# Kernel tuning notes

Hardware: AMD Instinct MI355X
Metric: run time of the kernel (lower is better)

Reference implementation:

```python
import jax, jax.numpy as jnp
import numpy as np

NUM_EXPERTS = 8
TOP_K = 2


def setup_inputs() -> dict:
    key = jax.random.key(0)
    k0, k1, k2, k3, k4 = jax.random.split(key, 5)
    T, D, F, E = 4096, 2048, 4096, NUM_EXPERTS  # tokens, hidden, intermediate, experts
    s_in = 1.0 / np.sqrt(D).astype(np.float32)
    s_mid = 1.0 / np.sqrt(F).astype(np.float32)
    return {
        "hidden_states": jax.random.normal(k0, (T, D), jnp.float32),
        "gate_w": jax.random.normal(k1, (D, E), jnp.float32) * s_in,   # router gate (no bias)
        "w1": jax.random.normal(k2, (E, D, F), jnp.float32) * s_in,     # expert gate proj
        "w3": jax.random.normal(k3, (E, D, F), jnp.float32) * s_in,     # expert up proj
        "w2": jax.random.normal(k4, (E, F, D), jnp.float32) * s_mid,    # expert down proj
    }


def reference(hidden_states, gate_w, w1, w3, w2):
    x = hidden_states  # [T, D] (original flattens any leading dims)
    # Router: logits in fp32 (router_logits.float()), softmax over ALL experts,
    # take top-k WITHOUT renormalization (renormalize=False).
    logits = (x @ gate_w).astype(jnp.float32)            # [T, E]
    probs = jax.nn.softmax(logits, axis=-1)              # [T, E]
    topk_w, topk_i = jax.lax.top_k(probs, TOP_K)         # [T, K]
    # Dense combine weights: zero for non-selected experts. [T, E]
    combine = jnp.sum(
        jax.nn.one_hot(topk_i, NUM_EXPERTS, dtype=x.dtype) * topk_w[..., None],
        axis=1,
    )

    # SwiGLU experts, vmapped over the expert axis (fixed, small E).
    def expert_fn(w1e, w3e, w2e):
        return (jax.nn.silu(x @ w1e) * (x @ w3e)) @ w2e  # [T, D]

    expert_out = jax.vmap(expert_fn)(w1, w3, w2)         # [E, T, D]
    return jnp.einsum("te,etd->td", combine, expert_out)  # [T, D]
```

## Files before the change

kernel.cpp:

```cpp
#include <hip/hip_runtime.h>
#include <hip/hip_bf16.h>

#define TK 4096
#define DD 2048
#define FF 4096
#define NE 8
#define BM 128
#define BN 128
#define BN2 256
#define BKR 32
#define BKP 64

typedef __attribute__((ext_vector_type(8))) short bf16x8;
typedef __attribute__((ext_vector_type(4))) short bf16x4;
typedef __attribute__((ext_vector_type(4))) float f32x4;

__device__ __forceinline__ unsigned short f2bf(float f) {
  return __builtin_bit_cast(unsigned short, __float2bfloat16(f));
}
__device__ __forceinline__ float bf2f(unsigned short u) {
  return __builtin_bit_cast(float, (unsigned)u << 16);
}

__device__ __forceinline__ void gl16(const unsigned short* g, unsigned short* l) {
  __builtin_amdgcn_global_load_lds(
      (const __attribute__((address_space(1))) unsigned int*)g,
      (__attribute__((address_space(3))) unsigned int*)l, 16, 0, 0);
}

#define VMCNT(n) asm volatile("s_waitcnt vmcnt(" #n ")" ::: "memory")
#define SBAR()   __builtin_amdgcn_s_barrier()

__device__ __forceinline__ int g_swz(int row) { return ((row >> 1) & 3) ^ ((row >> 3) & 3); }
__device__ __forceinline__ int swzoff(int row, int bir) {
  return row * 64 + ((((bir >> 4) ^ g_swz(row)) & 3) << 4) + (bir & 15);
}
__device__ __forceinline__ int permB(int f) {
  return (f & 0x60) | ((f & 3) << 3) | ((f >> 2) & 7);
}

__global__ void k_router(const float* __restrict__ x, const float* __restrict__ gw,
                         int* __restrict__ cnt, int* __restrict__ ltok,
                         float* __restrict__ lw, unsigned short* __restrict__ xb,
                         int2* __restrict__ t2s) {
  int tok = (blockIdx.x * blockDim.x + threadIdx.x) >> 6;
  int lane = threadIdx.x & 63;
  if (tok >= TK) return;
  const float* xr = x + (size_t)tok * DD;
  float a0=0,a1=0,a2=0,a3=0,a4=0,a5=0,a6=0,a7=0;
  for (int p = 0; p < DD / 256; ++p) {
    int d0 = p * 256 + lane * 4;
    f32x4 xv = *(const f32x4*)(xr + d0);
    if (xb) {
      bf16x4 t;
      t[0] = (short)f2bf(xv[0]); t[1] = (short)f2bf(xv[1]);
      t[2] = (short)f2bf(xv[2]); t[3] = (short)f2bf(xv[3]);
      *(bf16x4*)(xb + (size_t)tok * DD + d0) = t;
    }
#pragma unroll
    for (int j = 0; j < 4; ++j) {
      float xs = xv[j];
      const f32x4* g = (const f32x4*)(gw + (size_t)(d0 + j) * NE);
      f32x4 g0 = g[0], g1 = g[1];
      a0 += xs * g0[0]; a1 += xs * g0[1]; a2 += xs * g0[2]; a3 += xs * g0[3];
      a4 += xs * g1[0]; a5 += xs * g1[1]; a6 += xs * g1[2]; a7 += xs * g1[3];
    }
  }
#pragma unroll
  for (int s = 32; s > 0; s >>= 1) {
    a0 += __shfl_xor(a0, s, 64); a1 += __shfl_xor(a1, s, 64);
    a2 += __shfl_xor(a2, s, 64); a3 += __shfl_xor(a3, s, 64);
    a4 += __shfl_xor(a4, s, 64); a5 += __shfl_xor(a5, s, 64);
    a6 += __shfl_xor(a6, s, 64); a7 += __shfl_xor(a7, s, 64);
  }
  if (lane == 0) {
    float p_[NE] = {a0, a1, a2, a3, a4, a5, a6, a7};
    float m = p_[0];
#pragma unroll
    for (int e = 1; e < NE; ++e) m = fmaxf(m, p_[e]);
    float ssum = 0.f;
#pragma unroll
    for (int e = 0; e < NE; ++e) { p_[e] = __expf(p_[e] - m); ssum += p_[e]; }
    float inv = 1.f / ssum;
    int i1 = 0; float b1 = p_[0];
#pragma unroll
    for (int e = 1; e < NE; ++e) if (p_[e] > b1) { b1 = p_[e]; i1 = e; }
    int i2 = -1; float b2 = -1.f;
#pragma unroll
    for (int e = 0; e < NE; ++e) if (e != i1 && p_[e] > b2) { b2 = p_[e]; i2 = e; }
    int s1 = atomicAdd(&cnt[i1], 1);
    ltok[i1 * TK + s1] = tok; lw[i1 * TK + s1] = b1 * inv;
    int s2 = atomicAdd(&cnt[i2], 1);
    ltok[i2 * TK + s2] = tok; lw[i2 * TK + s2] = b2 * inv;
    if (t2s) t2s[tok] = make_int2(i1 * TK + s1, i2 * TK + s2);
  }
}

__global__ void k_prefix(const int* __restrict__ cnt, int* __restrict__ off) {
  if (threadIdx.x == 0) {
    int a = 0;
#pragma unroll
    for (int e = 0; e < NE; ++e) { off[e] = a; a += cnt[e]; }
    off[NE] = a;
  }
}

__global__ __launch_bounds__(256)
void k_tr(const float* __restrict__ src0, unsigned short* __restrict__ dst0,
          int R, int C) {
  const int e = blockIdx.z;
  const float* src = src0 + (size_t)e * R * C;
  unsigned short* dst = dst0 + (size_t)e * R * C;
  const int tid = threadIdx.x;
  const int w = tid >> 6, lane = tid & 63;
  const int r0 = blockIdx.y * 256 + w * 64 + (lane >> 3) * 8;
  const int c0 = blockIdx.x * 32 + (lane & 7) * 4;
  f32x4 v[8];
#pragma unroll
  for (int j = 0; j < 8; ++j) v[j] = *(const f32x4*)(src + (size_t)(r0 + j) * C + c0);
#pragma unroll
  for (int jc = 0; jc < 4; ++jc) {
    bf16x8 o;
#pragma unroll
    for (int j = 0; j < 8; ++j) o[j] = (short)f2bf(v[j][jc]);
    *(bf16x8*)(dst + (size_t)(c0 + jc) * R + r0) = o;
  }
}

__global__ __launch_bounds__(256)
void k_comb(const unsigned short* __restrict__ O, const int2* __restrict__ t2s,
            const int* __restrict__ off, float* __restrict__ out) {
  const int idx = blockIdx.x * 256 + threadIdx.x;
  const int t = idx >> 8;
  const int d0 = (idx & 255) * 8;
  const int2 v = t2s[t];
  const int s1 = off[v.x >> 12] + (v.x & (TK - 1));
  const int s2 = off[v.y >> 12] + (v.y & (TK - 1));
  bf16x8 a = *(const bf16x8*)(O + (size_t)s1 * DD + d0);
  bf16x8 b = *(const bf16x8*)(O + (size_t)s2 * DD + d0);
  f32x4 r0, r1;
#pragma unroll
  for (int j = 0; j < 4; ++j) {
    r0[j] = bf2f((unsigned short)a[j]) + bf2f((unsigned short)b[j]);
    r1[j] = bf2f((unsigned short)a[j + 4]) + bf2f((unsigned short)b[j + 4]);
  }
  float* o = out + (size_t)t * DD + d0;
  *(f32x4*)o = r0;
  *(f32x4*)(o + 4) = r1;
}


__global__ __launch_bounds__(256, 2)
void k_gemm1g(const unsigned short* __restrict__ xb, const unsigned short* __restrict__ w1t,
              const unsigned short* __restrict__ w3t, const int* __restrict__ cnt,
              const int* __restrict__ off, const int* __restrict__ ltok,
              const float* __restrict__ lw, unsigned short* __restrict__ H) {
  const int e = blockIdx.z;
  const int ce = cnt[e];
  const int m0 = blockIdx.y * BM;
  if (m0 >= ce) return;
  const int n0 = blockIdx.x * BN;
  const int tid = threadIdx.x, lane = tid & 63, w = tid >> 6;
  const int wr = w >> 1, wc = w & 1;
  const unsigned short* W1 = w1t + (size_t)e * FF * DD;
  const unsigned short* W3 = w3t + (size_t)e * FF * DD;
  const int base = off[e];

  __shared__ __align__(16) unsigned short As[BM * BKP];
  __shared__ __align__(16) unsigned short B1s[2][BM * BKP];
  __shared__ __align__(16) unsigned short B3s[2][BM * BKP];

  const int swz8 = ((lane & 7) ^ ((lane >> 3) & 7)) * 8;
  const unsigned short *aSrc[4], *b1Src[4], *b3Src[4];
#pragma unroll
  for (int i = 0; i < 4; ++i) {
    int row = w * 32 + i * 8 + (lane >> 3);
    int gm = m0 + row;
    int tok = (gm < ce) ? ltok[e * TK + gm] : ltok[e * TK];
    aSrc[i]  = xb + (size_t)tok * DD + swz8;
    b1Src[i] = W1 + (size_t)(n0 + row) * DD + swz8;
    b3Src[i] = W3 + (size_t)(n0 + row) * DD + swz8;
  }

  const int kc = lane >> 4;
  int aOff[4][2], bOff[4][2];
#pragma unroll
  for (int m = 0; m < 4; ++m) {
    int row = wr * 64 + m * 16 + (lane & 15);
#pragma unroll
    for (int kk = 0; kk < 2; ++kk) {
      int c = kk * 4 + kc;
      aOff[m][kk] = row * 128 + ((c ^ (row & 7)) << 4);
    }
  }
#pragma unroll
  for (int n = 0; n < 4; ++n) {
    int row = wc * 64 + n * 16 + (lane & 15);
#pragma unroll
    for (int kk = 0; kk < 2; ++kk) {
      int c = kk * 4 + kc;
      bOff[n][kk] = row * 128 + ((c ^ (row & 7)) << 4);
    }
  }

  f32x4 acc1[4][4], acc3[4][4];
#pragma unroll
  for (int m = 0; m < 4; ++m)
#pragma unroll
    for (int n = 0; n < 4; ++n)
#pragma unroll
      for (int j = 0; j < 4; ++j) { acc1[m][n][j] = 0.f; acc3[m][n][j] = 0.f; }

  auto STAGE_A = [&]() {
#pragma unroll
    for (int i = 0; i < 4; ++i) {
      gl16(aSrc[i], &As[(w * 4 + i) * 512]);
      aSrc[i] += BKP;
    }
  };
  auto STAGE_B = [&](int buf) {
#pragma unroll
    for (int i = 0; i < 4; ++i) {
      const int seg = w * 4 + i;
      gl16(b1Src[i], &B1s[buf][seg * 512]);
      gl16(b3Src[i], &B3s[buf][seg * 512]);
      b1Src[i] += BKP; b3Src[i] += BKP;
    }
  };
  auto COMPUTE = [&](int buf) {
#pragma unroll
    for (int kk = 0; kk < 2; ++kk) {
      bf16x8 af[4];
#pragma unroll
      for (int m = 0; m < 4; ++m) af[m] = *(const bf16x8*)((const char*)As + aOff[m][kk]);
#pragma unroll
      for (int n = 0; n < 4; ++n) {
        bf16x8 b1 = *(const bf16x8*)((const char*)B1s[buf] + bOff[n][kk]);
        bf16x8 b3 = *(const bf16x8*)((const char*)B3s[buf] + bOff[n][kk]);
#pragma unroll
        for (int m = 0; m < 4; ++m) {
          acc1[m][n] = __builtin_amdgcn_mfma_f32_16x16x32_bf16(af[m], b1, acc1[m][n], 0, 0, 0);
          acc3[m][n] = __builtin_amdgcn_mfma_f32_16x16x32_bf16(af[m], b3, acc3[m][n], 0, 0, 0);
        }
      }
    }
  };

  const int NT = DD / BKP;
  STAGE_A();
  STAGE_B(0);
  int b = 0;
  for (int kt = 0; kt < NT - 1; ++kt) {
    STAGE_B(b ^ 1);
    VMCNT(8);
    SBAR();
    COMPUTE(b);
    SBAR();
    STAGE_A();
    b ^= 1;
  }
  VMCNT(0);
  SBAR();
  COMPUTE(b);

#pragma unroll
  for (int m = 0; m < 4; ++m) {
    const int rbase = wr * 64 + m * 16 + ((lane >> 4) << 2);
    float wts[4]; bool val[4];
#pragma unroll
    for (int j = 0; j < 4; ++j) {
      int r = m0 + rbase + j;
      val[j] = r < ce;
      wts[j] = val[j] ? lw[e * TK + r] : 0.f;
    }
#pragma unroll
    for (int n = 0; n < 4; ++n) {
      const int col = n0 + wc * 64 + n * 16 + (lane & 15);
#pragma unroll
      for (int j = 0; j < 4; ++j) {
        if (!val[j]) continue;
        float s1 = acc1[m][n][j], s3 = acc3[m][n][j];
        float h = s1 / (1.f + __expf(-s1)) * s3 * wts[j];
        H[(size_t)(base + m0 + rbase + j) * FF + col] = f2bf(h);
      }
    }
  }
}

__global__ __launch_bounds__(256, 2)
void k_gemm2g(const unsigned short* __restrict__ H, const unsigned short* __restrict__ w2t,
              const int* __restrict__ cnt, const int* __restrict__ off,
              unsigned short* __restrict__ O) {
  const int e = blockIdx.z;
  const int ce = cnt[e];
  const int m0 = blockIdx.y * BM;
  if (m0 >= ce) return;
  const int n0 = blockIdx.x * BN2;
  const int tid = threadIdx.x, lane = tid & 63, w = tid >> 6;
  const int wr = w >> 1, wc = w & 1;
  const unsigned short* W2 = w2t + (size_t)e * DD * FF;
  const int base = off[e];

  __shared__ __align__(16) unsigned short As[BM * BKP];
  __shared__ __align__(16) unsigned short Bs[2][BN2 * BKP];

  const int swz8 = ((lane & 7) ^ ((lane >> 3) & 7)) * 8;
  const unsigned short *aSrc[4], *bSrc[8];
#pragma unroll
  for (int i = 0; i < 4; ++i) {
    int row = w * 32 + i * 8 + (lane >> 3);
    int gm = m0 + row;
    int hr = (gm < ce) ? gm : 0;
    aSrc[i] = H + (size_t)(base + hr) * FF + swz8;
  }
#pragma unroll
  for (int i = 0; i < 8; ++i) {
    int row = w * 64 + i * 8 + (lane >> 3);
    bSrc[i] = W2 + (size_t)(n0 + row) * FF + swz8;
  }

  const int kc = lane >> 4;
  int aOff[4][2], bOff[8][2];
#pragma unroll
  for (int m = 0; m < 4; ++m) {
    int row = wr * 64 + m * 16 + (lane & 15);
#pragma unroll
    for (int kk = 0; kk < 2; ++kk) {
      int c = kk * 4 + kc;
      aOff[m][kk] = row * 128 + ((c ^ (row & 7)) << 4);
    }
  }
#pragma unroll
  for (int n = 0; n < 8; ++n) {
    int row = wc * 128 + n * 16 + (lane & 15);
#pragma unroll
    for (int kk = 0; kk < 2; ++kk) {
      int c = kk * 4 + kc;
      bOff[n][kk] = row * 128 + ((c ^ (row & 7)) << 4);
    }
  }

  f32x4 acc[4][8];
#pragma unroll
  for (int m = 0; m < 4; ++m)
#pragma unroll
    for (int n = 0; n < 8; ++n)
#pragma unroll
      for (int j = 0; j < 4; ++j) acc[m][n][j] = 0.f;

  auto STAGE_A = [&]() {
#pragma unroll
    for (int i = 0; i < 4; ++i) {
      gl16(aSrc[i], &As[(w * 4 + i) * 512]);
      aSrc[i] += BKP;
    }
  };
  auto STAGE_B = [&](int buf) {
#pragma unroll
    for (int i = 0; i < 8; ++i) {
      gl16(bSrc[i], &Bs[buf][(w * 8 + i) * 512]);
      bSrc[i] += BKP;
    }
  };
  auto COMPUTE = [&](int buf) {
#pragma unroll
    for (int kk = 0; kk < 2; ++kk) {
      bf16x8 af[4];
#pragma unroll
      for (int m = 0; m < 4; ++m) af[m] = *(const bf16x8*)((const char*)As + aOff[m][kk]);
#pragma unroll
      for (int n = 0; n < 8; ++n) {
        bf16x8 bf = *(const bf16x8*)((const char*)Bs[buf] + bOff[n][kk]);
#pragma unroll
        for (int m = 0; m < 4; ++m)
          acc[m][n] = __builtin_amdgcn_mfma_f32_16x16x32_bf16(af[m], bf, acc[m][n], 0, 0, 0);
      }
    }
  };

  const int NT = FF / BKP;
  STAGE_A();
  STAGE_B(0);
  int b = 0;
  for (int kt = 0; kt < NT - 1; ++kt) {
    STAGE_B(b ^ 1);
    VMCNT(8);
    SBAR();
    COMPUTE(b);
    SBAR();
    STAGE_A();
    b ^= 1;
  }
  VMCNT(0);
  SBAR();
  COMPUTE(b);

#pragma unroll
  for (int m = 0; m < 4; ++m) {
    const int rbase = wr * 64 + m * 16 + ((lane >> 4) << 2);
#pragma unroll
    for (int n = 0; n < 8; ++n) {
      const int col = n0 + wc * 128 + n * 16 + (lane & 15);
#pragma unroll
      for (int j = 0; j < 4; ++j) {
        int r = m0 + rbase + j;
        if (r < ce) O[(size_t)(base + r) * DD + col] = f2bf(acc[m][n][j]);
      }
    }
  }
}

__global__ __launch_bounds__(256, 2)
void k_gemm1(const float* __restrict__ x, const float* __restrict__ w1g,
             const float* __restrict__ w3g, const int* __restrict__ cnt,
             const int* __restrict__ off, const int* __restrict__ ltok,
             const float* __restrict__ lw, unsigned short* __restrict__ H) {
  const int e = blockIdx.z;
  const int ce = cnt[e];
  const int m0 = blockIdx.y * BM;
  if (m0 >= ce) return;
  const int n0 = blockIdx.x * BN;
  const int tid = threadIdx.x, lane = tid & 63, wv = tid >> 6;
  const int wr = wv >> 1, wc = wv & 1;
  const float* W1 = w1g + (size_t)e * DD * FF;
  const float* W3 = w3g + (size_t)e * DD * FF;
  const int base = off[e];

  __shared__ unsigned short As[2][BM * BKR];
  __shared__ unsigned short B1s[2][BN * BKR];
  __shared__ unsigned short B3s[2][BN * BKR];

  const int arow = tid >> 1, ah = tid & 1;
  const float* xrow = (m0 + arow < ce) ? (x + (size_t)ltok[e * TK + (m0 + arow)] * DD) : nullptr;
  const int dblk = tid >> 5, fblk = tid & 31;

  const int kb = (lane >> 4) * 16;
  int aOff[4], bOff[4], wAoff[4], wBoff[4];
#pragma unroll
  for (int m = 0; m < 4; ++m) aOff[m] = swzoff(wr * 64 + m * 16 + (lane & 15), kb);
#pragma unroll
  for (int n = 0; n < 4; ++n) bOff[n] = swzoff(permB(wc * 64 + n * 16 + (lane & 15)), kb);
#pragma unroll
  for (int j = 0; j < 4; ++j) {
    wAoff[j] = swzoff(arow, ah * 32 + j * 8);
    wBoff[j] = swzoff(permB(fblk * 4 + j), dblk * 8);
  }

  f32x4 acc1[4][4], acc3[4][4];
#pragma unroll
  for (int m = 0; m < 4; ++m)
#pragma unroll
    for (int n = 0; n < 4; ++n)
#pragma unroll
      for (int j = 0; j < 4; ++j) { acc1[m][n][j] = 0.f; acc3[m][n][j] = 0.f; }

  f32x4 av[4], v1[4], v3[4];

  auto LOAD = [&](int kt) {
    const int k0 = kt * BKR;
#pragma unroll
    for (int j = 0; j < 4; ++j) {
      if (xrow) av[j] = *(const f32x4*)(xrow + k0 + ah * 16 + j * 4);
      else { av[j][0] = 0.f; av[j][1] = 0.f; av[j][2] = 0.f; av[j][3] = 0.f; }
    }
    const float* p1 = W1 + (size_t)(k0 + dblk * 4) * FF + (n0 + fblk * 4);
    const float* p3 = W3 + (size_t)(k0 + dblk * 4) * FF + (n0 + fblk * 4);
#pragma unroll
    for (int r = 0; r < 4; ++r) {
      v1[r] = *(const f32x4*)(p1 + (size_t)r * FF);
      v3[r] = *(const f32x4*)(p3 + (size_t)r * FF);
    }
  };
  auto STORE = [&](int buf) {
#pragma unroll
    for (int j = 0; j < 4; ++j) {
      bf16x4 t;
      t[0] = (short)f2bf(av[j][0]); t[1] = (short)f2bf(av[j][1]);
      t[2] = (short)f2bf(av[j][2]); t[3] = (short)f2bf(av[j][3]);
      *(bf16x4*)((char*)As[buf] + wAoff[j]) = t;
    }
#pragma unroll
    for (int j = 0; j < 4; ++j) {
      bf16x4 t1, t3;
      t1[0] = (short)f2bf(v1[0][j]); t1[1] = (short)f2bf(v1[1][j]);
      t1[2] = (short)f2bf(v1[2][j]); t1[3] = (short)f2bf(v1[3][j]);
      t3[0] = (short)f2bf(v3[0][j]); t3[1] = (short)f2bf(v3[1][j]);
      t3[2] = (short)f2bf(v3[2][j]); t3[3] = (short)f2bf(v3[3][j]);
      *(bf16x4*)((char*)B1s[buf] + wBoff[j]) = t1;
      *(bf16x4*)((char*)B3s[buf] + wBoff[j]) = t3;
    }
  };

  LOAD(0); STORE(0);
  int cur = 0;
  const int NT = DD / BKR;
  for (int kt = 0; kt < NT; ++kt) {
    if (kt + 1 < NT) LOAD(kt + 1);
    __syncthreads();
    bf16x8 af[4];
#pragma unroll
    for (int m = 0; m < 4; ++m) af[m] = *(const bf16x8*)((const char*)As[cur] + aOff[m]);
#pragma unroll
    for (int n = 0; n < 4; ++n) {
      bf16x8 b1 = *(const bf16x8*)((const char*)B1s[cur] + bOff[n]);
      bf16x8 b3 = *(const bf16x8*)((const char*)B3s[cur] + bOff[n]);
#pragma unroll
      for (int m = 0; m < 4; ++m) {
        acc1[m][n] = __builtin_amdgcn_mfma_f32_16x16x32_bf16(af[m], b1, acc1[m][n], 0, 0, 0);
        acc3[m][n] = __builtin_amdgcn_mfma_f32_16x16x32_bf16(af[m], b3, acc3[m][n], 0, 0, 0);
      }
    }
    if (kt + 1 < NT) STORE(cur ^ 1);
    cur ^= 1;
  }

#pragma unroll
  for (int m = 0; m < 4; ++m) {
    const int rbase = wr * 64 + m * 16 + ((lane >> 4) << 2);
    float wts[4]; bool val[4];
#pragma unroll
    for (int j = 0; j < 4; ++j) {
      int r = m0 + rbase + j;
      val[j] = r < ce;
      wts[j] = val[j] ? lw[e * TK + r] : 0.f;
    }
#pragma unroll
    for (int n = 0; n < 4; ++n) {
      const int col = n0 + wc * 64 + n * 16 + (lane & 15);
#pragma unroll
      for (int j = 0; j < 4; ++j) {
        if (!val[j]) continue;
        float s1 = acc1[m][n][j], s3 = acc3[m][n][j];
        float h = s1 / (1.f + __expf(-s1)) * s3 * wts[j];
        H[(size_t)(base + m0 + rbase + j) * FF + col] = f2bf(h);
      }
    }
  }
}

__global__ __launch_bounds__(256, 2)
void k_gemm2(const unsigned short* __restrict__ H, const float* __restrict__ w2g,
             const int* __restrict__ cnt, const int* __restrict__ off,
             const int* __restrict__ ltok, float* __restrict__ out) {
  const int e = blockIdx.z;
  const int ce = cnt[e];
  const int m0 = blockIdx.y * BM;
  if (m0 >= ce) return;
  const int n0 = blockIdx.x * BN;
  const int tid = threadIdx.x, lane = tid & 63, wv = tid >> 6;
  const int wr = wv >> 1, wc = wv & 1;
  const float* W2 = w2g + (size_t)e * FF * DD;
  const int base = off[e];

  __shared__ unsigned short As[2][BM * BKR];
  __shared__ unsigned short Bs[2][BN * BKR];

  const int arow = tid >> 1, ah = tid & 1;
  const bool aval = (m0 + arow) < ce;
  const unsigned short* hrow = H + (size_t)(base + m0 + arow) * FF;
  const int kblk = tid >> 5, nblk = tid & 31;

  const int kb = (lane >> 4) * 16;
  int aOff[4], bOff[4], wAoff[2], wBoff[4];
#pragma unroll
  for (int m = 0; m < 4; ++m) aOff[m] = swzoff(wr * 64 + m * 16 + (lane & 15), kb);
#pragma unroll
  for (int n = 0; n < 4; ++n) bOff[n] = swzoff(permB(wc * 64 + n * 16 + (lane & 15)), kb);
#pragma unroll
  for (int j = 0; j < 2; ++j) wAoff[j] = swzoff(arow, ah * 32 + j * 16);
#pragma unroll
  for (int j = 0; j < 4; ++j) wBoff[j] = swzoff(permB(nblk * 4 + j), kblk * 8);

  f32x4 acc[4][4];
#pragma unroll
  for (int m = 0; m < 4; ++m)
#pragma unroll
    for (int n = 0; n < 4; ++n)
#pragma unroll
      for (int j = 0; j < 4; ++j) acc[m][n][j] = 0.f;

  bf16x8 av2[2];
  f32x4 wv2[4];

  auto LOAD = [&](int kt) {
    const int k0 = kt * BKR;
#pragma unroll
    for (int j = 0; j < 2; ++j) {
      if (aval) av2[j] = *(const bf16x8*)(hrow + k0 + ah * 16 + j * 8);
      else {
#pragma unroll
        for (int q = 0; q < 8; ++q) av2[j][q] = 0;
      }
    }
    const float* p = W2 + (size_t)(k0 + kblk * 4) * DD + (n0 + nblk * 4);
#pragma unroll
    for (int r = 0; r < 4; ++r) wv2[r] = *(const f32x4*)(p + (size_t)r * DD);
  };
  auto STORE = [&](int buf) {
#pragma unroll
    for (int j = 0; j < 2; ++j) *(bf16x8*)((char*)As[buf] + wAoff[j]) = av2[j];
#pragma unroll
    for (int j = 0; j < 4; ++j) {
      bf16x4 t;
      t[0] = (short)f2bf(wv2[0][j]); t[1] = (short)f2bf(wv2[1][j]);
      t[2] = (short)f2bf(wv2[2][j]); t[3] = (short)f2bf(wv2[3][j]);
      *(bf16x4*)((char*)Bs[buf] + wBoff[j]) = t;
    }
  };

  LOAD(0); STORE(0);
  int cur = 0;
  const int NT = FF / BKR;
  for (int kt = 0; kt < NT; ++kt) {
    if (kt + 1 < NT) LOAD(kt + 1);
    __syncthreads();
    bf16x8 af[4];
#pragma unroll
    for (int m = 0; m < 4; ++m) af[m] = *(const bf16x8*)((const char*)As[cur] + aOff[m]);
#pragma unroll
    for (int n = 0; n < 4; ++n) {
      bf16x8 bf = *(const bf16x8*)((const char*)Bs[cur] + bOff[n]);
#pragma unroll
      for (int m = 0; m < 4; ++m)
        acc[m][n] = __builtin_amdgcn_mfma_f32_16x16x32_bf16(af[m], bf, acc[m][n], 0, 0, 0);
    }
    if (kt + 1 < NT) STORE(cur ^ 1);
    cur ^= 1;
  }

#pragma unroll
  for (int m = 0; m < 4; ++m) {
    const int rbase = wr * 64 + m * 16 + ((lane >> 4) << 2);
    int toks[4]; bool val[4];
#pragma unroll
    for (int j = 0; j < 4; ++j) {
      int r = m0 + rbase + j;
      val[j] = r < ce;
      toks[j] = val[j] ? ltok[e * TK + r] : 0;
    }
#pragma unroll
    for (int n = 0; n < 4; ++n) {
      const int col = n0 + wc * 64 + n * 16 + (lane & 15);
#pragma unroll
      for (int j = 0; j < 4; ++j)
        if (val[j]) atomicAdd(out + (size_t)toks[j] * DD + col, acc[m][n][j]);
    }
  }
}

extern "C" void kernel_launch(void* const* d_in, const int* in_sizes, int n_in,
                              void* d_out, int out_size, void* d_ws, size_t ws_size,
                              hipStream_t stream) {
  const float* x  = (const float*)d_in[0];
  const float* gw = (const float*)d_in[1];
  const float* w1 = (const float*)d_in[2];
  const float* w3 = (const float*)d_in[3];
  const float* w2 = (const float*)d_in[4];
  float* out = (float*)d_out;

  char* ws = (char*)d_ws;
  int*   cnt  = (int*)(ws);
  int*   off  = (int*)(ws + 64);
  int*   ltok = (int*)(ws + 256);
  float* lw   = (float*)(ws + 256 + (size_t)NE * TK * 4);
  int2*  t2s  = (int2*)(ws + 512 * 1024);

  const size_t SZ_XB = (size_t)TK * DD * 2;
  const size_t SZ_W  = (size_t)NE * DD * FF * 2;
  const size_t SZ_H  = (size_t)2 * TK * FF * 2;
  size_t o = (size_t)1 << 20;
  unsigned short* xb  = (unsigned short*)(ws + o); o += SZ_XB;
  unsigned short* w1t = (unsigned short*)(ws + o); o += SZ_W;
  unsigned short* w3t = (unsigned short*)(ws + o); o += SZ_W;
  unsigned short* w2t = (unsigned short*)(ws + o); o += SZ_W;
  unsigned short* Hg  = (unsigned short*)(ws + o); o += SZ_H;
  unsigned short* O   = w1t;
  const bool full = (ws_size >= o);

  hipMemsetAsync(cnt, 0, 64, stream);

  if (full) {
    k_router<<<dim3(TK / 4), 256, 0, stream>>>(x, gw, cnt, ltok, lw, xb, t2s);
    k_prefix<<<dim3(1), 64, 0, stream>>>(cnt, off);
    k_tr<<<dim3(FF / 32, DD / 256, NE), 256, 0, stream>>>(w1, w1t, DD, FF);
    k_tr<<<dim3(FF / 32, DD / 256, NE), 256, 0, stream>>>(w3, w3t, DD, FF);
    k_tr<<<dim3(DD / 32, FF / 256, NE), 256, 0, stream>>>(w2, w2t, FF, DD);
    k_gemm1g<<<dim3(FF / BN, TK / BM, NE), 256, 0, stream>>>(xb, w1t, w3t, cnt, off, ltok, lw, Hg);
    k_gemm2g<<<dim3(DD / BN2, TK / BM, NE), 256, 0, stream>>>(Hg, w2t, cnt, off, O);
    k_comb<<<dim3(TK * DD / 8 / 256), 256, 0, stream>>>(O, t2s, off, out);
  } else {
    unsigned short* H = (unsigned short*)(ws + ((size_t)1 << 20));
    if (ws_size < ((size_t)1 << 20) + SZ_H) return;
    hipMemsetAsync(d_out, 0, (size_t)out_size * 4, stream);
    k_router<<<dim3(TK / 4), 256, 0, stream>>>(x, gw, cnt, ltok, lw,
                                               (unsigned short*)nullptr, (int2*)nullptr);
    k_prefix<<<dim3(1), 64, 0, stream>>>(cnt, off);
    k_gemm1<<<dim3(FF / BN, TK / BM, NE), 256, 0, stream>>>(x, w1, w3, cnt, off, ltok, lw, H);
    k_gemm2<<<dim3(DD / BN, TK / BM, NE), 256, 0, stream>>>(H, w2, cnt, off, ltok, out);
  }
}
```

Baseline: 976.6 us.

## Interleave w1/w3 into one weight matrix and use a 256x256 gate-up GEMM tile

The weight transpose now writes w1 and w3 into one buffer, interleaved in 16-row groups. This lets the first expert GEMM treat gate and up projections as one matrix with N = 2F. The new kernel uses 512 threads and a 256x256 tile with K split into two 32-wide halves and double buffering. Loads are issued between MFMA groups with raised wave priority so memory traffic overlaps compute and the A tile is reused across more columns. The cost is more shared memory and registers per block, plus a tighter barrier and vmcnt schedule whose correctness depends on the exact interleave mapping in the epilogue.

```diff
diff --git a/kernel.cpp b/kernel.cpp
--- a/kernel.cpp
+++ b/kernel.cpp
@@ -30,6 +30,7 @@
 
 #define VMCNT(n) asm volatile("s_waitcnt vmcnt(" #n ")" ::: "memory")
 #define SBAR()   __builtin_amdgcn_s_barrier()
+#define MFMA_(a, b, c) __builtin_amdgcn_mfma_f32_16x16x32_bf16(a, b, c, 0, 0, 0)
 
 __device__ __forceinline__ int g_swz(int row) { return ((row >> 1) & 3) ^ ((row >> 3) & 3); }
 __device__ __forceinline__ int swzoff(int row, int bir) {
@@ -107,10 +108,10 @@
 
 __global__ __launch_bounds__(256)
 void k_tr(const float* __restrict__ src0, unsigned short* __restrict__ dst0,
-          int R, int C) {
+          int R, int C, int mode) {
   const int e = blockIdx.z;
   const float* src = src0 + (size_t)e * R * C;
-  unsigned short* dst = dst0 + (size_t)e * R * C;
+  unsigned short* dst = dst0 + (size_t)e * R * C * (mode ? 2 : 1);
   const int tid = threadIdx.x;
   const int w = tid >> 6, lane = tid & 63;
   const int r0 = blockIdx.y * 256 + w * 64 + (lane >> 3) * 8;
@@ -123,7 +124,9 @@
     bf16x8 o;
 #pragma unroll
     for (int j = 0; j < 8; ++j) o[j] = (short)f2bf(v[j][jc]);
-    *(bf16x8*)(dst + (size_t)(c0 + jc) * R + r0) = o;
+    int f = c0 + jc;
+    int rr = mode ? (((f >> 4) << 5) + ((mode - 1) << 4) + (f & 15)) : f;
+    *(bf16x8*)(dst + (size_t)rr * R + r0) = o;
   }
 }
 
@@ -149,139 +152,149 @@
   *(f32x4*)(o + 4) = r1;
 }
 
-
-__global__ __launch_bounds__(256, 2)
-void k_gemm1g(const unsigned short* __restrict__ xb, const unsigned short* __restrict__ w1t,
-              const unsigned short* __restrict__ w3t, const int* __restrict__ cnt,
-              const int* __restrict__ off, const int* __restrict__ ltok,
-              const float* __restrict__ lw, unsigned short* __restrict__ H) {
+__global__ __launch_bounds__(512, 2)
+void k_gemm1p(const unsigned short* __restrict__ xb, const unsigned short* __restrict__ w13t,
+              const int* __restrict__ cnt, const int* __restrict__ off,
+              const int* __restrict__ ltok, const float* __restrict__ lw,
+              unsigned short* __restrict__ H) {
   const int e = blockIdx.z;
   const int ce = cnt[e];
-  const int m0 = blockIdx.y * BM;
+  const int m0 = blockIdx.y * 256;
   if (m0 >= ce) return;
-  const int n0 = blockIdx.x * BN;
+  const int n0 = blockIdx.x * 256;
   const int tid = threadIdx.x, lane = tid & 63, w = tid >> 6;
-  const int wr = w >> 1, wc = w & 1;
-  const unsigned short* W1 = w1t + (size_t)e * FF * DD;
-  const unsigned short* W3 = w3t + (size_t)e * FF * DD;
+  const int wm = w >> 2, wn = w & 3;
+  const unsigned short* W = w13t + (size_t)e * 2 * FF * DD;
   const int base = off[e];
 
-  __shared__ __align__(16) unsigned short As[BM * BKP];
-  __shared__ __align__(16) unsigned short B1s[2][BM * BKP];
-  __shared__ __align__(16) unsigned short B3s[2][BM * BKP];
-
-  const int swz8 = ((lane & 7) ^ ((lane >> 3) & 7)) * 8;
-  const unsigned short *aSrc[4], *b1Src[4], *b3Src[4];
-#pragma unroll
-  for (int i = 0; i < 4; ++i) {
-    int row = w * 32 + i * 8 + (lane >> 3);
+  __shared__ __align__(16) unsigned short As[2][2][256 * 32];
+  __shared__ __align__(16) unsigned short Bs[2][2][256 * 32];
+
+  const int presw = ((lane & 3) ^ ((lane >> 3) & 3)) * 8;
+  const unsigned short *aSrc[2], *bSrc[2];
+#pragma unroll
+  for (int i = 0; i < 2; ++i) {
+    int row = i * 128 + w * 16 + (lane >> 2);
     int gm = m0 + row;
     int tok = (gm < ce) ? ltok[e * TK + gm] : ltok[e * TK];
-    aSrc[i]  = xb + (size_t)tok * DD + swz8;
-    b1Src[i] = W1 + (size_t)(n0 + row) * DD + swz8;
-    b3Src[i] = W3 + (size_t)(n0 + row) * DD + swz8;
-  }
-
-  const int kc = lane >> 4;
-  int aOff[4][2], bOff[4][2];
-#pragma unroll
-  for (int m = 0; m < 4; ++m) {
-    int row = wr * 64 + m * 16 + (lane & 15);
-#pragma unroll
-    for (int kk = 0; kk < 2; ++kk) {
-      int c = kk * 4 + kc;
-      aOff[m][kk] = row * 128 + ((c ^ (row & 7)) << 4);
-    }
+    aSrc[i] = xb + (size_t)tok * DD + presw;
+    bSrc[i] = W + (size_t)(n0 + row) * DD + presw;
+  }
+  const int ldsrow = (w * 16) * 32;
+
+  const int c = lane >> 4;
+  int aOff[8], bOff[4];
+#pragma unroll
+  for (int m = 0; m < 8; ++m) {
+    int r = wm * 128 + m * 16 + (lane & 15);
+    aOff[m] = r * 64 + ((c ^ ((r >> 1) & 3)) << 4);
   }
 #pragma unroll
   for (int n = 0; n < 4; ++n) {
-    int row = wc * 64 + n * 16 + (lane & 15);
-#pragma unroll
-    for (int kk = 0; kk < 2; ++kk) {
-      int c = kk * 4 + kc;
-      bOff[n][kk] = row * 128 + ((c ^ (row & 7)) << 4);
-    }
-  }
-
-  f32x4 acc1[4][4], acc3[4][4];
-#pragma unroll
-  for (int m = 0; m < 4; ++m)
+    int r = wn * 64 + n * 16 + (lane & 15);
+    bOff[n] = r * 64 + ((c ^ ((r >> 1) & 3)) << 4);
+  }
+
+  f32x4 acc[8][4];
+#pragma unroll
+  for (int m = 0; m < 8; ++m)
 #pragma unroll
     for (int n = 0; n < 4; ++n)
 #pragma unroll
-      for (int j = 0; j < 4; ++j) { acc1[m][n][j] = 0.f; acc3[m][n][j] = 0.f; }
-
-  auto STAGE_A = [&]() {
-#pragma unroll
-    for (int i = 0; i < 4; ++i) {
-      gl16(aSrc[i], &As[(w * 4 + i) * 512]);
-      aSrc[i] += BKP;
-    }
-  };
-  auto STAGE_B = [&](int buf) {
-#pragma unroll
-    for (int i = 0; i < 4; ++i) {
-      const int seg = w * 4 + i;
-      gl16(b1Src[i], &B1s[buf][seg * 512]);
-      gl16(b3Src[i], &B3s[buf][seg * 512]);
-      b1Src[i] += BKP; b3Src[i] += BKP;
-    }
-  };
-  auto COMPUTE = [&](int buf) {
-#pragma unroll
-    for (int kk = 0; kk < 2; ++kk) {
-      bf16x8 af[4];
-#pragma unroll
-      for (int m = 0; m < 4; ++m) af[m] = *(const bf16x8*)((const char*)As + aOff[m][kk]);
-#pragma unroll
-      for (int n = 0; n < 4; ++n) {
-        bf16x8 b1 = *(const bf16x8*)((const char*)B1s[buf] + bOff[n][kk]);
-        bf16x8 b3 = *(const bf16x8*)((const char*)B3s[buf] + bOff[n][kk]);
-#pragma unroll
-        for (int m = 0; m < 4; ++m) {
-          acc1[m][n] = __builtin_amdgcn_mfma_f32_16x16x32_bf16(af[m], b1, acc1[m][n], 0, 0, 0);
-          acc3[m][n] = __builtin_amdgcn_mfma_f32_16x16x32_bf16(af[m], b3, acc3[m][n], 0, 0, 0);
+      for (int j = 0; j < 4; ++j) acc[m][n][j] = 0.f;
+
+  auto SA = [&](int buf, int kh) {
+#pragma unroll
+    for (int i = 0; i < 2; ++i)
+      gl16(aSrc[i] + kh * 32, &As[buf][kh][ldsrow + i * 128 * 32]);
+  };
+  auto SB = [&](int buf, int kh) {
+#pragma unroll
+    for (int i = 0; i < 2; ++i)
+      gl16(bSrc[i] + kh * 32, &Bs[buf][kh][ldsrow + i * 128 * 32]);
+  };
+
+  SA(0, 0); SB(0, 0); SA(0, 1); SB(0, 1);
+  aSrc[0] += BKP; aSrc[1] += BKP; bSrc[0] += BKP; bSrc[1] += BKP;
+  VMCNT(4);
+  SBAR();
+
+  const int NT = DD / BKP;
+  int buf = 0;
+  bf16x8 afr[8], bfA, bfB;
+  for (int kt = 0; kt < NT; ++kt) {
+    const char* A0 = (const char*)As[buf][0];
+    const char* A1 = (const char*)As[buf][1];
+    const char* B0 = (const char*)Bs[buf][0];
+    const char* B1 = (const char*)Bs[buf][1];
+#pragma unroll
+    for (int m = 0; m < 8; ++m) afr[m] = *(const bf16x8*)(A0 + aOff[m]);
+    bfA = *(const bf16x8*)(B0 + bOff[0]);
+    bfB = *(const bf16x8*)(B0 + bOff[1]);
+    SA(buf ^ 1, 0);
+    __builtin_amdgcn_s_setprio(1);
+#pragma unroll
+    for (int m = 0; m < 8; ++m) {
+      acc[m][0] = MFMA_(afr[m], bfA, acc[m][0]);
+      acc[m][1] = MFMA_(afr[m], bfB, acc[m][1]);
+    }
+    __builtin_amdgcn_s_setprio(0);
+    SBAR();
+    bfA = *(const bf16x8*)(B0 + bOff[2]);
+    bfB = *(const bf16x8*)(B0 + bOff[3]);
+    SB(buf ^ 1, 0);
+    __builtin_amdgcn_s_setprio(1);
+#pragma unroll
+    for (int m = 0; m < 8; ++m) {
+      acc[m][2] = MFMA_(afr[m], bfA, acc[m][2]);
+      acc[m][3] = MFMA_(afr[m], bfB, acc[m][3]);
+    }
+    __builtin_amdgcn_s_setprio(0);
+    VMCNT(4);
+    SBAR();
+#pragma unroll
+    for (int m = 0; m < 8; ++m) afr[m] = *(const bf16x8*)(A1 + aOff[m]);
+    bfA = *(const bf16x8*)(B1 + bOff[0]);
+    bfB = *(const bf16x8*)(B1 + bOff[1]);
+    SA(buf ^ 1, 1);
+    __builtin_amdgcn_s_setprio(1);
+#pragma unroll
+    for (int m = 0; m < 8; ++m) {
+      acc[m][0] = MFMA_(afr[m], bfA, acc[m][0]);
+      acc[m][1] = MFMA_(afr[m], bfB, acc[m][1]);
+    }
+    __builtin_amdgcn_s_setprio(0);
+    SBAR();
+    bfA = *(const bf16x8*)(B1 + bOff[2]);
+    bfB = *(const bf16x8*)(B1 + bOff[3]);
+    SB(buf ^ 1, 1);
+    __builtin_amdgcn_s_setprio(1);
+#pragma unroll
+    for (int m = 0; m < 8; ++m) {
+      acc[m][2] = MFMA_(afr[m], bfA, acc[m][2]);
+      acc[m][3] = MFMA_(afr[m], bfB, acc[m][3]);
+    }
+    __builtin_amdgcn_s_setprio(0);
+    VMCNT(4);
+    SBAR();
+    aSrc[0] += BKP; aSrc[1] += BKP; bSrc[0] += BKP; bSrc[1] += BKP;
+    buf ^= 1;
+  }
+
+#pragma unroll
+  for (int m = 0; m < 8; ++m) {
+    const int rl = wm * 128 + m * 16 + ((lane >> 4) << 2);
+#pragma unroll
+    for (int p = 0; p < 2; ++p) {
+      const int fcol = ((n0 + wn * 64) >> 1) + p * 16 + (lane & 15);
+#pragma unroll
+      for (int j = 0; j < 4; ++j) {
+        int r = m0 + rl + j;
+        if (r < ce) {
+          float s1 = acc[m][2 * p][j], s3 = acc[m][2 * p + 1][j];
+          float h = s1 / (1.f + __expf(-s1)) * s3 * lw[e * TK + r];
+          H[(size_t)(base + r) * FF + fcol] = f2bf(h);
         }
-      }
-    }
-  };
-
-  const int NT = DD / BKP;
-  STAGE_A();
-  STAGE_B(0);
-  int b = 0;
-  for (int kt = 0; kt < NT - 1; ++kt) {
-    STAGE_B(b ^ 1);
-    VMCNT(8);
-    SBAR();
-    COMPUTE(b);
-    SBAR();
-    STAGE_A();
-    b ^= 1;
-  }
-  VMCNT(0);
-  SBAR();
-  COMPUTE(b);
-
-#pragma unroll
-  for (int m = 0; m < 4; ++m) {
-    const int rbase = wr * 64 + m * 16 + ((lane >> 4) << 2);
-    float wts[4]; bool val[4];
-#pragma unroll
-    for (int j = 0; j < 4; ++j) {
-      int r = m0 + rbase + j;
-      val[j] = r < ce;
-      wts[j] = val[j] ? lw[e * TK + r] : 0.f;
-    }
-#pragma unroll
-    for (int n = 0; n < 4; ++n) {
-      const int col = n0 + wc * 64 + n * 16 + (lane & 15);
-#pragma unroll
-      for (int j = 0; j < 4; ++j) {
-        if (!val[j]) continue;
-        float s1 = acc1[m][n][j], s3 = acc3[m][n][j];
-        float h = s1 / (1.f + __expf(-s1)) * s3 * wts[j];
-        H[(size_t)(base + m0 + rbase + j) * FF + col] = f2bf(h);
       }
     }
   }
@@ -326,8 +339,8 @@
     int row = wr * 64 + m * 16 + (lane & 15);
 #pragma unroll
     for (int kk = 0; kk < 2; ++kk) {
-      int c = kk * 4 + kc;
-      aOff[m][kk] = row * 128 + ((c ^ (row & 7)) << 4);
+      int cc = kk * 4 + kc;
+      aOff[m][kk] = row * 128 + ((cc ^ (row & 7)) << 4);
     }
   }
 #pragma unroll
@@ -335,8 +348,8 @@
     int row = wc * 128 + n * 16 + (lane & 15);
 #pragma unroll
     for (int kk = 0; kk < 2; ++kk) {
-      int c = kk * 4 + kc;
-      bOff[n][kk] = row * 128 + ((c ^ (row & 7)) << 4);
+      int cc = kk * 4 + kc;
+      bOff[n][kk] = row * 128 + ((cc ^ (row & 7)) << 4);
     }
   }
 
@@ -665,16 +678,16 @@
   float* lw   = (float*)(ws + 256 + (size_t)NE * TK * 4);
   int2*  t2s  = (int2*)(ws + 512 * 1024);
 
-  const size_t SZ_XB = (size_t)TK * DD * 2;
-  const size_t SZ_W  = (size_t)NE * DD * FF * 2;
-  const size_t SZ_H  = (size_t)2 * TK * FF * 2;
+  const size_t SZ_XB  = (size_t)TK * DD * 2;
+  const size_t SZ_W13 = (size_t)NE * 2 * FF * DD * 2;
+  const size_t SZ_W   = (size_t)NE * DD * FF * 2;
+  const size_t SZ_H   = (size_t)2 * TK * FF * 2;
   size_t o = (size_t)1 << 20;
-  unsigned short* xb  = (unsigned short*)(ws + o); o += SZ_XB;
-  unsigned short* w1t = (unsigned short*)(ws + o); o += SZ_W;
-  unsigned short* w3t = (unsigned short*)(ws + o); o += SZ_W;
-  unsigned short* w2t = (unsigned short*)(ws + o); o += SZ_W;
-  unsigned short* Hg  = (unsigned short*)(ws + o); o += SZ_H;
-  unsigned short* O   = w1t;
+  unsigned short* xb   = (unsigned short*)(ws + o); o += SZ_XB;
+  unsigned short* w13t = (unsigned short*)(ws + o); o += SZ_W13;
+  unsigned short* w2t  = (unsigned short*)(ws + o); o += SZ_W;
+  unsigned short* Hg   = (unsigned short*)(ws + o); o += SZ_H;
+  unsigned short* O    = w13t;
   const bool full = (ws_size >= o);
 
   hipMemsetAsync(cnt, 0, 64, stream);
@@ -682,10 +695,10 @@
   if (full) {
     k_router<<<dim3(TK / 4), 256, 0, stream>>>(x, gw, cnt, ltok, lw, xb, t2s);
     k_prefix<<<dim3(1), 64, 0, stream>>>(cnt, off);
-    k_tr<<<dim3(FF / 32, DD / 256, NE), 256, 0, stream>>>(w1, w1t, DD, FF);
-    k_tr<<<dim3(FF / 32, DD / 256, NE), 256, 0, stream>>>(w3, w3t, DD, FF);
-    k_tr<<<dim3(DD / 32, FF / 256, NE), 256, 0, stream>>>(w2, w2t, FF, DD);
-    k_gemm1g<<<dim3(FF / BN, TK / BM, NE), 256, 0, stream>>>(xb, w1t, w3t, cnt, off, ltok, lw, Hg);
+    k_tr<<<dim3(FF / 32, DD / 256, NE), 256, 0, stream>>>(w1, w13t, DD, FF, 1);
+    k_tr<<<dim3(FF / 32, DD / 256, NE), 256, 0, stream>>>(w3, w13t, DD, FF, 2);
+    k_tr<<<dim3(DD / 32, FF / 256, NE), 256, 0, stream>>>(w2, w2t, FF, DD, 0);
+    k_gemm1p<<<dim3(2 * FF / 256, TK / 256, NE), 512, 0, stream>>>(xb, w13t, cnt, off, ltok, lw, Hg);
     k_gemm2g<<<dim3(DD / BN2, TK / BM, NE), 256, 0, stream>>>(Hg, w2t, cnt, off, O);
     k_comb<<<dim3(TK * DD / 8 / 256), 256, 0, stream>>>(O, t2s, off, out);
   } else {
```

Result: slower. 999.1 us (+2.3%).
